# Kernel optimization log

Measured on AMD Instinct MI355X. Metric: run time of the kernel, lower is better.

The kernel has to match this reference:

```python
import jax, jax.numpy as jnp
import numpy as np

D_MODEL = 1024
D_FF = 1024
NUM_EXPERTS = 8
TOP_K = 2


def setup_inputs() -> dict:
    key = jax.random.key(0)
    ks = jax.random.split(key, 5)
    s_in = 1.0 / np.sqrt(D_MODEL)
    s_ff = 1.0 / np.sqrt(D_FF)
    return {
        "x": jax.random.normal(ks[0], (4, 2048, D_MODEL), dtype=jnp.float32),
        "gate_w": jax.random.normal(ks[1], (NUM_EXPERTS, D_MODEL), dtype=jnp.float32) * s_in,
        # torch Linear weight layout: [out_features, in_features], stacked over experts
        "w_gate": jax.random.normal(ks[2], (NUM_EXPERTS, D_FF, D_MODEL), dtype=jnp.float32) * s_in,
        "w_up": jax.random.normal(ks[3], (NUM_EXPERTS, D_FF, D_MODEL), dtype=jnp.float32) * s_in,
        "w_down": jax.random.normal(ks[4], (NUM_EXPERTS, D_MODEL, D_FF), dtype=jnp.float32) * s_ff,
    }


def reference(x, gate_w, w_gate, w_up, w_down):
    B, S, D = x.shape
    T = B * S
    E = gate_w.shape[0]
    xt = x.reshape(T, D)

    # Router
    logits = xt @ gate_w.T                      # [T, E]
    probs = jax.nn.softmax(logits, axis=-1)
    top_v, top_i = jax.lax.top_k(probs, TOP_K)  # [T, K]
    top_v = top_v / jnp.sum(top_v, axis=-1, keepdims=True)

    tokens_per_expert = jnp.sum(jax.nn.one_hot(top_i, E, dtype=jnp.float32), axis=(0, 1))  # [E]
    f = tokens_per_expert / jnp.sum(tokens_per_expert)
    P = jnp.mean(probs, axis=0)
    aux_loss = E * jnp.sum(f * P)

    # Combine weights: per-token weight for each expert (sum over top-k slots)
    combine = jnp.zeros((T, E), dtype=x.dtype).at[jnp.arange(T)[:, None], top_i].add(top_v)  # [T, E]

    # Dense per-expert SwiGLU (equivalent math to masked gather/scatter loop)
    g = jnp.einsum('td,efd->etf', xt, w_gate)   # [E, T, F]
    u = jnp.einsum('td,efd->etf', xt, w_up)     # [E, T, F]
    act = jax.nn.silu(g) * u
    eo = jnp.einsum('etf,edf->etd', act, w_down)  # [E, T, D]

    out = jnp.einsum('te,etd->td', combine, eo).reshape(B, S, D)
    return out, aux_loss, tokens_per_expert
```

## Files before the change

### kernel.cpp

```cpp
#include <hip/hip_runtime.h>


#define T_TOK   8192
#define DM      1024
#define DFF     1024
#define NE      8
#define CAP     16384
#define R1_BLK  (T_TOK / 4)

typedef __attribute__((ext_vector_type(8))) short bf16x8;
typedef __attribute__((ext_vector_type(4))) float f32x4;

#define ASYNC16(gp, lp) __builtin_amdgcn_global_load_lds( \
    (const __attribute__((address_space(1))) unsigned int*)(gp), \
    (__attribute__((address_space(3))) unsigned int*)(lp), 16, 0, 0)

__device__ __forceinline__ unsigned short f2bf(float f) {
    union { float f; unsigned u; } c; c.f = f;
    unsigned r = c.u + 0x7fffu + ((c.u >> 16) & 1u);
    return (unsigned short)(r >> 16);
}
__device__ __forceinline__ float bf2f(unsigned short h) {
    union { unsigned u; float f; } c; c.u = ((unsigned)h) << 16;
    return c.f;
}

__global__ __launch_bounds__(256) void cvt3_kernel(
    const float* __restrict__ s0, const float* __restrict__ s1, const float* __restrict__ s2,
    unsigned short* __restrict__ d0, unsigned short* __restrict__ d1, unsigned short* __restrict__ d2)
{
    int idx = blockIdx.x * 256 + threadIdx.x;
    int seg = idx >> 21;
    int off = (idx & ((1 << 21) - 1)) * 4;
    const float* s = (seg == 0) ? s0 : (seg == 1) ? s1 : s2;
    unsigned short* d = (seg == 0) ? d0 : (seg == 1) ? d1 : d2;
    float4 v = *(const float4*)(s + off);
    ushort4 o;
    o.x = f2bf(v.x); o.y = f2bf(v.y); o.z = f2bf(v.z); o.w = f2bf(v.w);
    *(ushort4*)(d + off) = o;
}

__global__ __launch_bounds__(256) void router_kernel(
    const float* __restrict__ x, const float* __restrict__ gate_w,
    unsigned short* __restrict__ xb,
    int* __restrict__ topi, float2* __restrict__ topw,
    float* __restrict__ psum_part)
{
    __shared__ float gw[NE * DM];
    __shared__ float blk_psum[NE];
    int tid = threadIdx.x;
    for (int i = tid; i < NE * DM; i += 256) gw[i] = gate_w[i];
    if (tid < NE) blk_psum[tid] = 0.f;
    __syncthreads();

    int wv = tid >> 6, lane = tid & 63;
    int t = blockIdx.x * 4 + wv;

    float acc[NE];
    #pragma unroll
    for (int e = 0; e < NE; ++e) acc[e] = 0.f;
    const float* xr = x + (size_t)t * DM;
    unsigned short* xbr = xb + (size_t)t * DM;
    #pragma unroll 4
    for (int i = 0; i < DM / 64; ++i) {
        float xv = xr[i * 64 + lane];
        xbr[i * 64 + lane] = f2bf(xv);
        #pragma unroll
        for (int e = 0; e < NE; ++e)
            acc[e] += xv * gw[e * DM + i * 64 + lane];
    }
    #pragma unroll
    for (int e = 0; e < NE; ++e) {
        float v = acc[e];
        #pragma unroll
        for (int s = 32; s > 0; s >>= 1) v += __shfl_xor(v, s, 64);
        acc[e] = v;
    }
    if (lane == 0) {
        float mx = acc[0];
        #pragma unroll
        for (int e = 1; e < NE; ++e) mx = fmaxf(mx, acc[e]);
        float p[NE], sum = 0.f;
        #pragma unroll
        for (int e = 0; e < NE; ++e) { p[e] = expf(acc[e] - mx); sum += p[e]; }
        float inv = 1.f / sum;
        #pragma unroll
        for (int e = 0; e < NE; ++e) { p[e] *= inv; atomicAdd(&blk_psum[e], p[e]); }
        int i1 = 0; float v1 = p[0];
        #pragma unroll
        for (int e = 1; e < NE; ++e) if (p[e] > v1) { v1 = p[e]; i1 = e; }
        int i2 = -1; float v2 = -1.f;
        #pragma unroll
        for (int e = 0; e < NE; ++e) { if (e == i1) continue; if (p[e] > v2) { v2 = p[e]; i2 = e; } }
        float winv = 1.f / (v1 + v2);
        topi[t] = i1 | (i2 << 8);
        topw[t] = make_float2(v1 * winv, v2 * winv);
    }
    __syncthreads();
    if (tid < NE) psum_part[blockIdx.x * NE + tid] = blk_psum[tid];
}

__global__ __launch_bounds__(256) void scatter_kernel(
    const int* __restrict__ topi,
    int* __restrict__ elist, int* __restrict__ ecnt)
{
    __shared__ int lcnt[NE];
    __shared__ int lbase[NE];
    int tid = threadIdx.x;
    if (tid < NE) lcnt[tid] = 0;
    __syncthreads();
    int t = blockIdx.x * 256 + tid;
    int pk = topi[t];
    int e1 = pk & 0xff, e2 = (pk >> 8) & 0xff;
    int p1 = atomicAdd(&lcnt[e1], 1);
    int p2 = atomicAdd(&lcnt[e2], 1);
    __syncthreads();
    if (tid < NE) lbase[tid] = atomicAdd(&ecnt[tid], lcnt[tid]);
    __syncthreads();
    elist[e1 * CAP + lbase[e1] + p1] = t * 2 + 0;
    elist[e2 * CAP + lbase[e2] + p2] = t * 2 + 1;
}

__global__ __launch_bounds__(256) void finalize_kernel(
    const int* __restrict__ ecnt, const float* __restrict__ psum_part,
    float* __restrict__ out_tail)
{
    __shared__ float red[256];
    __shared__ float parts[NE];
    int tid = threadIdx.x;
    int e = tid & 7, b0 = tid >> 3;
    float s = 0.f;
    for (int b = b0; b < R1_BLK; b += 32) s += psum_part[b * NE + e];
    red[tid] = s;
    __syncthreads();
    if (tid < NE) {
        float tot = 0.f;
        #pragma unroll
        for (int j = 0; j < 32; ++j) tot += red[tid + NE * j];
        float P = tot / (float)T_TOK;
        float f = (float)ecnt[tid] / (float)(2 * T_TOK);
        parts[tid] = f * P;
        out_tail[1 + tid] = (float)ecnt[tid];
    }
    __syncthreads();
    if (tid == 0) {
        float s2 = 0.f;
        for (int i = 0; i < NE; ++i) s2 += parts[i];
        out_tail[0] = (float)NE * s2;
    }
}

__global__ __launch_bounds__(256) void gemm1_kernel(
    const unsigned short* __restrict__ xb,
    const unsigned short* __restrict__ wgb,
    const unsigned short* __restrict__ wub,
    const int* __restrict__ elist, const int* __restrict__ ecnt,
    unsigned short* __restrict__ Hbuf)
{
    int e = blockIdx.z, mt = blockIdx.y, ft = blockIdx.x;
    int ne = ecnt[e];
    if (mt * 128 >= ne) return;

    __shared__ unsigned short As[128 * 64];
    __shared__ unsigned short Gs[64 * 64];
    __shared__ unsigned short Us[64 * 64];
    __shared__ int tsafe[128];
    __shared__ int rawts[128];

    int tid = threadIdx.x;
    if (tid < 128) {
        int pos = mt * 128 + tid;
        int ts0 = elist[e * CAP + mt * 128];
        int ts = (pos < ne) ? elist[e * CAP + pos] : ts0;
        tsafe[tid] = ts >> 1;
        rawts[tid] = (pos < ne) ? ts : -1;
    }
    __syncthreads();

    int wave = tid >> 6, lane = tid & 63;
    int quad = lane >> 4, col = lane & 15;
    int cr = tid >> 3;
    int cl = ((tid & 7) ^ (cr & 7)) * 8;

    const size_t woff = (size_t)e * (size_t)DFF * DM;
    const unsigned short* ap[4];
    #pragma unroll
    for (int j = 0; j < 4; ++j) ap[j] = xb + (size_t)tsafe[j * 32 + cr] * DM + cl;
    const unsigned short* gp[2];
    const unsigned short* up[2];
    #pragma unroll
    for (int j = 0; j < 2; ++j) {
        gp[j] = wgb + woff + (size_t)(ft * 64 + j * 32 + cr) * DM + cl;
        up[j] = wub + woff + (size_t)(ft * 64 + j * 32 + cr) * DM + cl;
    }
    unsigned short* lA = As + wave * 512;
    unsigned short* lG = Gs + wave * 512;
    unsigned short* lU = Us + wave * 512;

    f32x4 accG[2][4], accU[2][4];
    #pragma unroll
    for (int i = 0; i < 2; ++i)
        #pragma unroll
        for (int n = 0; n < 4; ++n) { accG[i][n] = (f32x4){0,0,0,0}; accU[i][n] = (f32x4){0,0,0,0}; }

    for (int k0 = 0; k0 < DM; k0 += 64) {
        __syncthreads();
        #pragma unroll
        for (int j = 0; j < 4; ++j) ASYNC16(ap[j] + k0, lA + j * 2048);
        #pragma unroll
        for (int j = 0; j < 2; ++j) {
            ASYNC16(gp[j] + k0, lG + j * 2048);
            ASYNC16(up[j] + k0, lU + j * 2048);
        }
        __syncthreads();
        #pragma unroll
        for (int ksoff = 0; ksoff < 8; ksoff += 4) {
            bf16x8 a[2], g[4], u[4];
            #pragma unroll
            for (int i = 0; i < 2; ++i) {
                int m = wave * 32 + i * 16 + col;
                a[i] = *(const bf16x8*)&As[m * 64 + ((quad + ksoff) ^ (m & 7)) * 8];
            }
            #pragma unroll
            for (int n = 0; n < 4; ++n) {
                int nb = n * 16 + col;
                int off = nb * 64 + ((quad + ksoff) ^ (nb & 7)) * 8;
                g[n] = *(const bf16x8*)&Gs[off];
                u[n] = *(const bf16x8*)&Us[off];
            }
            #pragma unroll
            for (int i = 0; i < 2; ++i)
                #pragma unroll
                for (int n = 0; n < 4; ++n) {
                    accG[i][n] = __builtin_amdgcn_mfma_f32_16x16x32_bf16(a[i], g[n], accG[i][n], 0, 0, 0);
                    accU[i][n] = __builtin_amdgcn_mfma_f32_16x16x32_bf16(a[i], u[n], accU[i][n], 0, 0, 0);
                }
        }
    }
    #pragma unroll
    for (int i = 0; i < 2; ++i) {
        #pragma unroll
        for (int r = 0; r < 4; ++r) {
            int row = wave * 32 + i * 16 + quad * 4 + r;
            int ts = rawts[row];
            if (ts < 0) continue;
            unsigned short* hr = Hbuf + (size_t)ts * DFF + ft * 64 + col;
            #pragma unroll
            for (int n = 0; n < 4; ++n) {
                float gg = accG[i][n][r], uu = accU[i][n][r];
                float h = (gg / (1.f + expf(-gg))) * uu;
                hr[n * 16] = f2bf(h);
            }
        }
    }
}

__global__ __launch_bounds__(256) void gemm2_kernel(
    const unsigned short* __restrict__ Hbuf,
    const unsigned short* __restrict__ wdb,
    const int* __restrict__ elist, const int* __restrict__ ecnt,
    unsigned short* __restrict__ eo)
{
    int e = blockIdx.z, mt = blockIdx.y, dt = blockIdx.x;
    int ne = ecnt[e];
    if (mt * 128 >= ne) return;

    __shared__ unsigned short As[128 * 64];
    __shared__ unsigned short Bs[128 * 64];
    __shared__ int tsafe[128];
    __shared__ int rawts[128];

    int tid = threadIdx.x;
    if (tid < 128) {
        int pos = mt * 128 + tid;
        int ts0 = elist[e * CAP + mt * 128];
        int ts = (pos < ne) ? elist[e * CAP + pos] : ts0;
        tsafe[tid] = ts;
        rawts[tid] = (pos < ne) ? ts : -1;
    }
    __syncthreads();

    int wave = tid >> 6, lane = tid & 63;
    int quad = lane >> 4, col = lane & 15;
    int wr = (wave >> 1) * 64, wc = (wave & 1) * 64;
    int cr = tid >> 3;
    int cl = ((tid & 7) ^ (cr & 7)) * 8;

    const size_t woff = (size_t)e * (size_t)DM * DFF;
    const unsigned short* ap[4];
    const unsigned short* bp[4];
    #pragma unroll
    for (int j = 0; j < 4; ++j) {
        ap[j] = Hbuf + (size_t)tsafe[j * 32 + cr] * DFF + cl;
        bp[j] = wdb + woff + (size_t)(dt * 128 + j * 32 + cr) * DFF + cl;
    }
    unsigned short* lA = As + wave * 512;
    unsigned short* lB = Bs + wave * 512;

    f32x4 acc[4][4];
    #pragma unroll
    for (int i = 0; i < 4; ++i)
        #pragma unroll
        for (int n = 0; n < 4; ++n) acc[i][n] = (f32x4){0,0,0,0};

    for (int k0 = 0; k0 < DFF; k0 += 64) {
        __syncthreads();
        #pragma unroll
        for (int j = 0; j < 4; ++j) {
            ASYNC16(ap[j] + k0, lA + j * 2048);
            ASYNC16(bp[j] + k0, lB + j * 2048);
        }
        __syncthreads();
        #pragma unroll
        for (int ksoff = 0; ksoff < 8; ksoff += 4) {
            bf16x8 a[4], b[4];
            #pragma unroll
            for (int i = 0; i < 4; ++i) {
                int m = wr + i * 16 + col;
                a[i] = *(const bf16x8*)&As[m * 64 + ((quad + ksoff) ^ (m & 7)) * 8];
            }
            #pragma unroll
            for (int n = 0; n < 4; ++n) {
                int nb = wc + n * 16 + col;
                b[n] = *(const bf16x8*)&Bs[nb * 64 + ((quad + ksoff) ^ (nb & 7)) * 8];
            }
            #pragma unroll
            for (int i = 0; i < 4; ++i)
                #pragma unroll
                for (int n = 0; n < 4; ++n)
                    acc[i][n] = __builtin_amdgcn_mfma_f32_16x16x32_bf16(a[i], b[n], acc[i][n], 0, 0, 0);
        }
    }
    #pragma unroll
    for (int i = 0; i < 4; ++i) {
        #pragma unroll
        for (int r = 0; r < 4; ++r) {
            int row = wr + i * 16 + quad * 4 + r;
            int ts = rawts[row];
            if (ts < 0) continue;
            unsigned short* er = eo + (size_t)ts * DM + dt * 128 + wc + col;
            #pragma unroll
            for (int n = 0; n < 4; ++n)
                er[n * 16] = f2bf(acc[i][n][r]);
        }
    }
}

__global__ __launch_bounds__(256) void combine_kernel(
    const unsigned short* __restrict__ eo, const float2* __restrict__ topw,
    float* __restrict__ out)
{
    int idx = blockIdx.x * 256 + threadIdx.x;
    int t = idx >> 7;
    int c = (idx & 127) << 3;
    float2 w = topw[t];
    const unsigned short* e0 = eo + (size_t)(t * 2) * DM + c;
    ushort4 a0 = *(const ushort4*)e0;
    ushort4 a1 = *(const ushort4*)(e0 + 4);
    ushort4 b0 = *(const ushort4*)(e0 + DM);
    ushort4 b1 = *(const ushort4*)(e0 + DM + 4);
    float* orow = out + (size_t)t * DM + c;
    float4 o0, o1;
    o0.x = w.x * bf2f(a0.x) + w.y * bf2f(b0.x);
    o0.y = w.x * bf2f(a0.y) + w.y * bf2f(b0.y);
    o0.z = w.x * bf2f(a0.z) + w.y * bf2f(b0.z);
    o0.w = w.x * bf2f(a0.w) + w.y * bf2f(b0.w);
    o1.x = w.x * bf2f(a1.x) + w.y * bf2f(b1.x);
    o1.y = w.x * bf2f(a1.y) + w.y * bf2f(b1.y);
    o1.z = w.x * bf2f(a1.z) + w.y * bf2f(b1.z);
    o1.w = w.x * bf2f(a1.w) + w.y * bf2f(b1.w);
    *(float4*)orow = o0;
    *(float4*)(orow + 4) = o1;
}

extern "C" void kernel_launch(void* const* d_in, const int* in_sizes, int n_in,
                              void* d_out, int out_size, void* d_ws, size_t ws_size,
                              hipStream_t stream) {
    const float* x      = (const float*)d_in[0];
    const float* gate_w = (const float*)d_in[1];
    const float* w_gate = (const float*)d_in[2];
    const float* w_up   = (const float*)d_in[3];
    const float* w_down = (const float*)d_in[4];
    float* out = (float*)d_out;

    char* p = (char*)d_ws;
    unsigned short* xb   = (unsigned short*)p; p += (size_t)T_TOK * DM * 2;
    unsigned short* wgb  = (unsigned short*)p; p += (size_t)NE * DFF * DM * 2;
    unsigned short* wub  = (unsigned short*)p; p += (size_t)NE * DFF * DM * 2;
    unsigned short* wdb  = (unsigned short*)p; p += (size_t)NE * DM * DFF * 2;
    unsigned short* Hbuf = (unsigned short*)p; p += (size_t)2 * T_TOK * DFF * 2;
    int*   elist = (int*)p;   p += (size_t)NE * CAP * 4;
    int*   ecnt  = (int*)p;   p += NE * 4;
    int*   topi  = (int*)p;   p += (size_t)T_TOK * 4;
    float2* topw = (float2*)p; p += (size_t)T_TOK * 8;
    float* psum_part = (float*)p; p += (size_t)R1_BLK * NE * 4;
    unsigned short* eo = wgb;

    hipMemsetAsync(ecnt, 0, NE * 4, stream);

    cvt3_kernel<<<3 * (NE * DFF * DM / 4) / 256, 256, 0, stream>>>(
        w_gate, w_up, w_down, wgb, wub, wdb);

    router_kernel<<<R1_BLK, 256, 0, stream>>>(x, gate_w, xb, topi, topw, psum_part);
    scatter_kernel<<<T_TOK / 256, 256, 0, stream>>>(topi, elist, ecnt);
    finalize_kernel<<<1, 256, 0, stream>>>(ecnt, psum_part, out + (size_t)T_TOK * DM);

    gemm1_kernel<<<dim3(DFF / 64, CAP / 128, NE), 256, 0, stream>>>(xb, wgb, wub, elist, ecnt, Hbuf);
    gemm2_kernel<<<dim3(DM / 128, CAP / 128, NE), 256, 0, stream>>>(Hbuf, wdb, elist, ecnt, eo);
    combine_kernel<<<T_TOK * DM / 8 / 256, 256, 0, stream>>>(eo, topw, out);
}
```

Before: 347.7 us.

## Fuse weight conversion, router, scatter and finalize into one kernel

Merges the weight fp32→bf16 conversion, router, expert scatter and aux-loss finalize into a single launch. Conversion blocks run alongside router blocks, and the last router block, found through an atomic counter, builds the expert lists serially and computes the aux loss. This removes three launches and the memset of ecnt and lets the conversion overlap with routing. In exchange, the scatter is now serialized in one block over 32 chunks, and every block carries the router's shared-memory footprint.

```diff
diff --git a/kernel.cpp b/kernel.cpp
--- a/kernel.cpp
+++ b/kernel.cpp
@@ -7,6 +7,7 @@
 #define NE      8
 #define CAP     16384
 #define R1_BLK  (T_TOK / 4)
+#define CVT_BLK 2048
 
 typedef __attribute__((ext_vector_type(8))) short bf16x8;
 typedef __attribute__((ext_vector_type(4))) float f32x4;
@@ -25,30 +26,40 @@
     return c.f;
 }
 
-__global__ __launch_bounds__(256) void cvt3_kernel(
+__global__ __launch_bounds__(256) void mega_kernel(
+    const float* __restrict__ x, const float* __restrict__ gate_w,
     const float* __restrict__ s0, const float* __restrict__ s1, const float* __restrict__ s2,
-    unsigned short* __restrict__ d0, unsigned short* __restrict__ d1, unsigned short* __restrict__ d2)
+    unsigned short* __restrict__ d0, unsigned short* __restrict__ d1, unsigned short* __restrict__ d2,
+    unsigned short* __restrict__ xb,
+    int* __restrict__ topi, float2* __restrict__ topw, float* __restrict__ psum_part,
+    int* __restrict__ elist, int* __restrict__ ecnt, int* __restrict__ rdone,
+    float* __restrict__ out_tail)
 {
-    int idx = blockIdx.x * 256 + threadIdx.x;
-    int seg = idx >> 21;
-    int off = (idx & ((1 << 21) - 1)) * 4;
-    const float* s = (seg == 0) ? s0 : (seg == 1) ? s1 : s2;
-    unsigned short* d = (seg == 0) ? d0 : (seg == 1) ? d1 : d2;
-    float4 v = *(const float4*)(s + off);
-    ushort4 o;
-    o.x = f2bf(v.x); o.y = f2bf(v.y); o.z = f2bf(v.z); o.w = f2bf(v.w);
-    *(ushort4*)(d + off) = o;
-}
-
-__global__ __launch_bounds__(256) void router_kernel(
-    const float* __restrict__ x, const float* __restrict__ gate_w,
-    unsigned short* __restrict__ xb,
-    int* __restrict__ topi, float2* __restrict__ topw,
-    float* __restrict__ psum_part)
-{
+    int tid = threadIdx.x;
+
+    if (blockIdx.x >= R1_BLK) {
+        int base = (blockIdx.x - R1_BLK) * 256 + tid;
+        #pragma unroll
+        for (int it = 0; it < 12; ++it) {
+            int idx = base + it * (CVT_BLK * 256);
+            int seg = idx >> 21;
+            int off = (idx & ((1 << 21) - 1)) * 4;
+            const float* s = (seg == 0) ? s0 : (seg == 1) ? s1 : s2;
+            unsigned short* d = (seg == 0) ? d0 : (seg == 1) ? d1 : d2;
+            float4 v = *(const float4*)(s + off);
+            ushort4 o;
+            o.x = f2bf(v.x); o.y = f2bf(v.y); o.z = f2bf(v.z); o.w = f2bf(v.w);
+            *(ushort4*)(d + off) = o;
+        }
+        return;
+    }
+
     __shared__ float gw[NE * DM];
     __shared__ float blk_psum[NE];
-    int tid = threadIdx.x;
+    __shared__ int lcnt[NE], rbase[NE], cb8[NE];
+    __shared__ float parts[NE];
+    __shared__ int lastflag;
+
     for (int i = tid; i < NE * DM; i += 256) gw[i] = gate_w[i];
     if (tid < NE) blk_psum[tid] = 0.f;
     __syncthreads();
@@ -98,39 +109,37 @@
     }
     __syncthreads();
     if (tid < NE) psum_part[blockIdx.x * NE + tid] = blk_psum[tid];
-}
-
-__global__ __launch_bounds__(256) void scatter_kernel(
-    const int* __restrict__ topi,
-    int* __restrict__ elist, int* __restrict__ ecnt)
-{
-    __shared__ int lcnt[NE];
-    __shared__ int lbase[NE];
-    int tid = threadIdx.x;
-    if (tid < NE) lcnt[tid] = 0;
-    __syncthreads();
-    int t = blockIdx.x * 256 + tid;
-    int pk = topi[t];
-    int e1 = pk & 0xff, e2 = (pk >> 8) & 0xff;
-    int p1 = atomicAdd(&lcnt[e1], 1);
-    int p2 = atomicAdd(&lcnt[e2], 1);
-    __syncthreads();
-    if (tid < NE) lbase[tid] = atomicAdd(&ecnt[tid], lcnt[tid]);
-    __syncthreads();
-    elist[e1 * CAP + lbase[e1] + p1] = t * 2 + 0;
-    elist[e2 * CAP + lbase[e2] + p2] = t * 2 + 1;
-}
-
-__global__ __launch_bounds__(256) void finalize_kernel(
-    const int* __restrict__ ecnt, const float* __restrict__ psum_part,
-    float* __restrict__ out_tail)
-{
-    __shared__ float red[256];
-    __shared__ float parts[NE];
-    int tid = threadIdx.x;
+
+    __threadfence();
+    if (tid == 0) lastflag = (atomicAdd(rdone, 1) == R1_BLK - 1) ? 1 : 0;
+    __syncthreads();
+    if (!lastflag) return;
+    __threadfence();
+
+    if (tid < NE) rbase[tid] = 0;
+    __syncthreads();
+    for (int ch = 0; ch < 32; ++ch) {
+        int tt = ch * 256 + tid;
+        int pk = topi[tt];
+        int e1 = pk & 0xff, e2 = (pk >> 8) & 0xff;
+        if (tid < NE) lcnt[tid] = 0;
+        __syncthreads();
+        int p1 = atomicAdd(&lcnt[e1], 1);
+        int p2 = atomicAdd(&lcnt[e2], 1);
+        __syncthreads();
+        if (tid < NE) { cb8[tid] = rbase[tid]; rbase[tid] += lcnt[tid]; }
+        __syncthreads();
+        elist[e1 * CAP + cb8[e1] + p1] = tt * 2 + 0;
+        elist[e2 * CAP + cb8[e2] + p2] = tt * 2 + 1;
+        __syncthreads();
+    }
+    if (tid < NE) ecnt[tid] = rbase[tid];
+
+    float* red = gw;
     int e = tid & 7, b0 = tid >> 3;
     float s = 0.f;
     for (int b = b0; b < R1_BLK; b += 32) s += psum_part[b * NE + e];
+    __syncthreads();
     red[tid] = s;
     __syncthreads();
     if (tid < NE) {
@@ -138,9 +147,9 @@
         #pragma unroll
         for (int j = 0; j < 32; ++j) tot += red[tid + NE * j];
         float P = tot / (float)T_TOK;
-        float f = (float)ecnt[tid] / (float)(2 * T_TOK);
+        float f = (float)rbase[tid] / (float)(2 * T_TOK);
         parts[tid] = f * P;
-        out_tail[1 + tid] = (float)ecnt[tid];
+        out_tail[1 + tid] = (float)rbase[tid];
     }
     __syncthreads();
     if (tid == 0) {
@@ -394,16 +403,15 @@
     int*   topi  = (int*)p;   p += (size_t)T_TOK * 4;
     float2* topw = (float2*)p; p += (size_t)T_TOK * 8;
     float* psum_part = (float*)p; p += (size_t)R1_BLK * NE * 4;
+    int*   rdone = (int*)p;   p += 64;
     unsigned short* eo = wgb;
 
-    hipMemsetAsync(ecnt, 0, NE * 4, stream);
-
-    cvt3_kernel<<<3 * (NE * DFF * DM / 4) / 256, 256, 0, stream>>>(
-        w_gate, w_up, w_down, wgb, wub, wdb);
-
-    router_kernel<<<R1_BLK, 256, 0, stream>>>(x, gate_w, xb, topi, topw, psum_part);
-    scatter_kernel<<<T_TOK / 256, 256, 0, stream>>>(topi, elist, ecnt);
-    finalize_kernel<<<1, 256, 0, stream>>>(ecnt, psum_part, out + (size_t)T_TOK * DM);
+    hipMemsetAsync(rdone, 0, 64, stream);
+
+    mega_kernel<<<R1_BLK + CVT_BLK, 256, 0, stream>>>(
+        x, gate_w, w_gate, w_up, w_down, wgb, wub, wdb,
+        xb, topi, topw, psum_part, elist, ecnt, rdone,
+        out + (size_t)T_TOK * DM);
 
     gemm1_kernel<<<dim3(DFF / 64, CAP / 128, NE), 256, 0, stream>>>(xb, wgb, wub, elist, ecnt, Hbuf);
     gemm2_kernel<<<dim3(DM / 128, CAP / 128, NE), 256, 0, stream>>>(Hbuf, wdb, elist, ecnt, eo);
```

Result: slower. 497.5 us (+43.1%).
